# Optimization experiments

Hardware: AMD Instinct MI355X
Metric: run time of the kernel (lower is better)

Reference implementation:

```python
import jax, jax.numpy as jnp
import numpy as np
from jax import lax

S, B, VIN, VOUT, U, E = 64, 256, 128, 128, 1024, 512
START_CODE = 0
T_DEC = 25  # MAX_DECODE_STEPS


def gru_step(x, h, Wih, Whh, bih, bhh):
    # PyTorch GRU cell, gate order r,z,n
    gi = x @ Wih.T + bih
    gh = h @ Whh.T + bhh
    ir, iz, inn = jnp.split(gi, 3, axis=-1)
    hr, hz, hn = jnp.split(gh, 3, axis=-1)
    r = jax.nn.sigmoid(ir + hr)
    z = jax.nn.sigmoid(iz + hz)
    n = jnp.tanh(inn + r * hn)
    return (1.0 - z) * n + z * h


def setup_inputs() -> dict:
    key = jax.random.key(0)
    ks = jax.random.split(key, 20)
    sc = 0.05
    inp = {
        'x': jax.random.normal(ks[0], (S, B, VIN), jnp.float32),
        'x_len': jnp.maximum(jnp.sort(jax.random.randint(ks[1], (B,), 0, S + 1)), 1),
        'enc_Wih': jax.random.normal(ks[2], (3 * U, VIN), jnp.float32) * sc,
        'enc_Whh': jax.random.normal(ks[3], (3 * U, U), jnp.float32) * sc,
        'enc_bih': jnp.zeros((3 * U,), jnp.float32),
        'enc_bhh': jnp.zeros((3 * U,), jnp.float32),
        'dec_Wih': jax.random.normal(ks[4], (3 * U, E + U), jnp.float32) * sc,
        'dec_Whh': jax.random.normal(ks[5], (3 * U, U), jnp.float32) * sc,
        'dec_bih': jnp.zeros((3 * U,), jnp.float32),
        'dec_bhh': jnp.zeros((3 * U,), jnp.float32),
        'o2h_W': jax.random.normal(ks[6], (E, VOUT), jnp.float32) * sc,
        'o2h_b': jnp.zeros((E,), jnp.float32),
        'fc_W': jax.random.normal(ks[7], (VOUT, U), jnp.float32) * sc,
        'fc_b': jnp.zeros((VOUT,), jnp.float32),
        'W1_W': jax.random.normal(ks[8], (U, U), jnp.float32) * sc,
        'W1_b': jnp.zeros((U,), jnp.float32),
        'W2_W': jax.random.normal(ks[9], (U, U), jnp.float32) * sc,
        'W2_b': jnp.zeros((U,), jnp.float32),
        'V_W': jax.random.normal(ks[10], (1, U), jnp.float32) * sc,
        'V_b': jnp.zeros((1,), jnp.float32),
    }
    return inp


def _forward(x, x_len, enc_Wih, enc_Whh, enc_bih, enc_bhh,
             dec_Wih, dec_Whh, dec_bih, dec_bhh,
             o2h_W, o2h_b, fc_W, fc_b, W1_W, W1_b, W2_W, W2_b, V_W, V_b):
    # ---- Encoder GRU with length masking (pack/pad semantics) ----
    h0 = jnp.zeros((B, U), jnp.float32)
    t_idx = jnp.arange(S)

    def enc_step(h, inp_t):
        xt, t = inp_t
        mask = (t < x_len)[:, None]  # [B,1]
        hn = gru_step(xt, h, enc_Wih, enc_Whh, enc_bih, enc_bhh)
        h = jnp.where(mask, hn, h)
        out = jnp.where(mask, hn, 0.0)
        return h, out

    enc_hidden, enc_out = lax.scan(enc_step, h0, (x, t_idx))  # enc_out [S,B,U]
    enc_out = jnp.transpose(enc_out, (1, 0, 2))  # [B,S,U]

    # ---- Greedy decode (teacher_force=False), 25 steps ----
    enc_proj = enc_out @ W1_W.T + W1_b  # precompute W1(enc_output), [B,S,U]
    start = jnp.zeros((B, VOUT), jnp.float32).at[:, START_CODE].set(1.0)

    def dec_step(carry, _):
        h, dec_in = carry
        score = jnp.tanh(enc_proj + (h @ W2_W.T + W2_b)[:, None, :])  # [B,S,U]
        logits = score @ V_W.T + V_b  # [B,S,1]
        attn = jax.nn.softmax(logits, axis=1)
        ctx = jnp.sum(attn * enc_out, axis=1)  # [B,U]
        emb = dec_in @ o2h_W.T + o2h_b  # [B,E]
        gx = jnp.concatenate([ctx, emb], axis=-1)
        hn = gru_step(gx, h, dec_Wih, dec_Whh, dec_bih, dec_bhh)
        pred = hn @ fc_W.T + fc_b  # [B,VOUT]
        onehot = jax.nn.one_hot(jnp.argmax(pred, axis=-1), VOUT, dtype=pred.dtype)
        return (hn, lax.stop_gradient(onehot)), pred

    _, preds = lax.scan(dec_step, (enc_hidden, start), None, length=T_DEC - 1)
    return jnp.concatenate([start[None], preds], axis=0)  # [25,B,VOUT]


def reference(x, x_len, enc_Wih, enc_Whh, enc_bih, enc_bhh,
              dec_Wih, dec_Whh, dec_bih, dec_bhh,
              o2h_W, o2h_b, fc_W, fc_b, W1_W, W1_b, W2_W, W2_b, V_W, V_b):
    return _forward(x, x_len, enc_Wih, enc_Whh, enc_bih, enc_bhh,
                    dec_Wih, dec_Whh, dec_bih, dec_bhh,
                    o2h_W, o2h_b, fc_W, fc_b, W1_W, W1_b, W2_W, W2_b, V_W, V_b)
```

## Files before the change

### kernel.cpp

```cpp
#include <hip/hip_runtime.h>
#include <math.h>

#define SLEN 64
#define BATCH 256
#define VIND 128
#define VOUTD 128
#define UDIM 1024
#define EDIM 512
#define TDEC 25
#define GXW 1536
#define U3 3072
#define NSEG 12

typedef __attribute__((ext_vector_type(8))) short short8;
typedef __attribute__((ext_vector_type(4))) float f32x4;

#define MFMA(acc, A, B) acc = __builtin_amdgcn_mfma_f32_16x16x32_bf16((A), (B), (acc), 0, 0, 0)

__device__ __forceinline__ float sigm(float x) { return 1.f / (1.f + expf(-x)); }

__device__ __forceinline__ float tanhf_fast(float x) {
    float ax = fabsf(x);
    float e = __expf(-2.f * ax);
    float t = (1.f - e) / (1.f + e);
    return copysignf(t, x);
}

__device__ __forceinline__ short f2bf(float f) {
    unsigned u = __float_as_uint(f);
    u += 0x7FFF + ((u >> 16) & 1);
    return (short)(u >> 16);
}
__device__ __forceinline__ float bf2f(short h) {
    return __uint_as_float(((unsigned)(unsigned short)h) << 16);
}

__device__ __forceinline__ size_t pkChunk(int r, int k, int K) {
    return ((size_t)(r >> 4) * (K >> 5) + (k >> 5)) * 64 + ((r & 15) + 16 * ((k >> 3) & 3));
}

union S8 { short s[8]; short8 v; };

__device__ __forceinline__ void writeSplit8(short* Hi, short* Lo, size_t chunk,
                                            const float* vals) {
    S8 h, l;
#pragma unroll
    for (int j = 0; j < 8; j++) {
        short hb = f2bf(vals[j]);
        h.s[j] = hb;
        l.s[j] = f2bf(vals[j] - bf2f(hb));
    }
    ((short8*)Hi)[chunk] = h.v;
    ((short8*)Lo)[chunk] = l.v;
}

__global__ void init_kernel(float* __restrict__ h0, short* __restrict__ hpHi,
                            short* __restrict__ hpLo, float* __restrict__ out0,
                            int* __restrict__ idx,
                            const float* __restrict__ o2h_W,
                            const float* __restrict__ o2h_b,
                            float* __restrict__ o2hT) {
    int i = blockIdx.x * 256 + threadIdx.x;
    if (i < BATCH * UDIM) { h0[i] = 0.f; hpHi[i] = 0; hpLo[i] = 0; }
    if (i < BATCH * VOUTD) out0[i] = ((i & (VOUTD - 1)) == 0) ? 1.f : 0.f;
    if (i < BATCH) idx[i] = 0;
    if (i < VOUTD * EDIM) {
        int v = i >> 9, e = i & (EDIM - 1);
        o2hT[i] = o2h_W[(size_t)e * VOUTD + v] + o2h_b[e];
    }
}

struct PackSeg {
    const float* sA; const float* sB;
    short* Hi; short* Lo;
    int KA, KB, offA, offB, chunkStart;
};
struct PackArgs { PackSeg s[NSEG]; };

__global__ void pack_all(PackArgs pa, int total) {
    int gid = blockIdx.x * 256 + threadIdx.x;
    if (gid >= total) return;
    int si = 0;
#pragma unroll
    for (int i = 1; i < NSEG; i++) si = (gid >= pa.s[i].chunkStart) ? i : si;
    PackSeg sg = pa.s[si];
    int local = gid - sg.chunkStart;
    int K = sg.KA + sg.KB;
    int cpr = K >> 3;
    int r = local / cpr, k0 = (local - r * cpr) * 8;
    const float* src = (k0 < sg.KA)
        ? sg.sA + (size_t)(sg.offA + r) * sg.KA + k0
        : sg.sB + (size_t)(sg.offB + r) * sg.KB + (k0 - sg.KA);
    float v[8];
#pragma unroll
    for (int j = 0; j < 8; j++) v[j] = src[j];
    writeSplit8(sg.Hi, sg.Lo, pkChunk(r, k0, K), v);
}

__global__ __launch_bounds__(256) void gemm_w(
    const short8* __restrict__ Ahi, const short8* __restrict__ Alo,
    const short8* __restrict__ Whi, const short8* __restrict__ Wlo,
    const float* __restrict__ bias, float* __restrict__ C,
    int KT, int N) {
    int tid = threadIdx.x, lane = tid & 63, wave = tid >> 6;
    int m16 = blockIdx.x * 4 + (wave & 1) * 2;
    int nb = blockIdx.y * 8 + (wave >> 1) * 4;
    const short8* a0h = Ahi + (size_t)m16 * KT * 64 + lane;
    const short8* a1h = a0h + (size_t)KT * 64;
    const short8* a0l = Alo + (size_t)m16 * KT * 64 + lane;
    const short8* a1l = a0l + (size_t)KT * 64;
    const short8* w0h = Whi + (size_t)(nb + 0) * KT * 64 + lane;
    const short8* w1h = Whi + (size_t)(nb + 1) * KT * 64 + lane;
    const short8* w2h = Whi + (size_t)(nb + 2) * KT * 64 + lane;
    const short8* w3h = Whi + (size_t)(nb + 3) * KT * 64 + lane;
    const short8* w0l = Wlo + (size_t)(nb + 0) * KT * 64 + lane;
    const short8* w1l = Wlo + (size_t)(nb + 1) * KT * 64 + lane;
    const short8* w2l = Wlo + (size_t)(nb + 2) * KT * 64 + lane;
    const short8* w3l = Wlo + (size_t)(nb + 3) * KT * 64 + lane;
    f32x4 acc0[4] = {}, acc1[4] = {};

    for (int kt = 0; kt < KT; kt++) {
        size_t o = (size_t)kt * 64;
        short8 A0H = a0h[o], A1H = a1h[o], A0L = a0l[o], A1L = a1l[o];
        short8 WH0 = w0h[o], WL0 = w0l[o];
        MFMA(acc0[0], A0H, WH0); MFMA(acc1[0], A1H, WH0);
        MFMA(acc0[0], A0H, WL0); MFMA(acc1[0], A1H, WL0);
        MFMA(acc0[0], A0L, WH0); MFMA(acc1[0], A1L, WH0);
        short8 WH1 = w1h[o], WL1 = w1l[o];
        MFMA(acc0[1], A0H, WH1); MFMA(acc1[1], A1H, WH1);
        MFMA(acc0[1], A0H, WL1); MFMA(acc1[1], A1H, WL1);
        MFMA(acc0[1], A0L, WH1); MFMA(acc1[1], A1L, WH1);
        short8 WH2 = w2h[o], WL2 = w2l[o];
        MFMA(acc0[2], A0H, WH2); MFMA(acc1[2], A1H, WH2);
        MFMA(acc0[2], A0H, WL2); MFMA(acc1[2], A1H, WL2);
        MFMA(acc0[2], A0L, WH2); MFMA(acc1[2], A1L, WH2);
        short8 WH3 = w3h[o], WL3 = w3l[o];
        MFMA(acc0[3], A0H, WH3); MFMA(acc1[3], A1H, WH3);
        MFMA(acc0[3], A0H, WL3); MFMA(acc1[3], A1H, WL3);
        MFMA(acc0[3], A0L, WH3); MFMA(acc1[3], A1L, WH3);
    }
    int rsub = (lane >> 4) * 4, cn = lane & 15;
    int row0 = (m16 + 0) * 16 + rsub;
    int row1 = (m16 + 1) * 16 + rsub;
#pragma unroll
    for (int j = 0; j < 4; j++) {
        int col = (nb + j) * 16 + cn;
        float bb = bias ? bias[col] : 0.f;
#pragma unroll
        for (int r = 0; r < 4; r++) {
            C[(size_t)(row0 + r) * N + col] = acc0[j][r] + bb;
            C[(size_t)(row1 + r) * N + col] = acc1[j][r] + bb;
        }
    }
}

__global__ __launch_bounds__(256) void gemm_bm32(
    const short8* __restrict__ Ahi, const short8* __restrict__ Alo,
    const short8* __restrict__ Whi, const short8* __restrict__ Wlo,
    const float* __restrict__ bias, float* __restrict__ C,
    int KT, int N) {
    int tid = threadIdx.x, lane = tid & 63, wave = tid >> 6;
    int m16 = blockIdx.x * 2 + (wave & 1);
    int n16 = blockIdx.y * 4 + (wave >> 1) * 2;
    const short8* ah = Ahi + (size_t)m16 * KT * 64 + lane;
    const short8* al = Alo + (size_t)m16 * KT * 64 + lane;
    const short8* w0h = Whi + (size_t)n16 * KT * 64 + lane;
    const short8* w1h = w0h + (size_t)KT * 64;
    const short8* w0l = Wlo + (size_t)n16 * KT * 64 + lane;
    const short8* w1l = w0l + (size_t)KT * 64;
    f32x4 a0 = {0,0,0,0}, a1 = {0,0,0,0};
    for (int kt = 0; kt < KT; kt++) {
        size_t o = (size_t)kt * 64;
        short8 AH = ah[o], AL = al[o];
        short8 W0H = w0h[o], W0L = w0l[o], W1H = w1h[o], W1L = w1l[o];
        MFMA(a0, AH, W0H); MFMA(a1, AH, W1H);
        MFMA(a0, AH, W0L); MFMA(a1, AH, W1L);
        MFMA(a0, AL, W0H); MFMA(a1, AL, W1H);
    }
    int rsub = (lane >> 4) * 4, cn = lane & 15;
    float b0 = bias ? bias[(n16 + 0) * 16 + cn] : 0.f;
    float b1 = bias ? bias[(n16 + 1) * 16 + cn] : 0.f;
#pragma unroll
    for (int r = 0; r < 4; r++) {
        int row = m16 * 16 + rsub + r;
        C[(size_t)row * N + (n16 + 0) * 16 + cn] = a0[r] + b0;
        C[(size_t)row * N + (n16 + 1) * 16 + cn] = a1[r] + b1;
    }
}

__global__ __launch_bounds__(384) void enc_gru3(
    const short8* __restrict__ hinH8, const short8* __restrict__ hinL8,
    const short8* __restrict__ WrH, const short8* __restrict__ WrL,
    const short8* __restrict__ WzH, const short8* __restrict__ WzL,
    const short8* __restrict__ WnH, const short8* __restrict__ WnL,
    const float* __restrict__ gi,
    const float* __restrict__ bih, const float* __restrict__ bhh,
    const float* __restrict__ hinF, float* __restrict__ houtF,
    short* __restrict__ hoH, short* __restrict__ hoL,
    short* __restrict__ eaHi, short* __restrict__ eaLo,
    const int* __restrict__ x_len, int t) {
    __shared__ float sC[6][2][16][16];
    __shared__ float sHo[2][16][16];
    __shared__ float sEo[2][16][16];
    int tid = threadIdx.x, lane = tid & 63, wave = tid >> 6;
    int g = blockIdx.x;
    int m16a = blockIdx.y * 2;
    int gate = wave >> 1, half = wave & 1;
    const short8* a0h = hinH8 + (size_t)m16a * 32 * 64 + (size_t)half * 16 * 64 + lane;
    const short8* a0l = hinL8 + (size_t)m16a * 32 * 64 + (size_t)half * 16 * 64 + lane;
    const short8* a1h = a0h + (size_t)32 * 64;
    const short8* a1l = a0l + (size_t)32 * 64;
    const short8* WH0 = (gate == 0) ? WrH : (gate == 1) ? WzH : WnH;
    const short8* WL0 = (gate == 0) ? WrL : (gate == 1) ? WzL : WnL;
    const short8* wh = WH0 + (size_t)g * 32 * 64 + (size_t)half * 16 * 64 + lane;
    const short8* wl = WL0 + (size_t)g * 32 * 64 + (size_t)half * 16 * 64 + lane;
    f32x4 acc0 = {0, 0, 0, 0}, acc1 = {0, 0, 0, 0};
    for (int kt = 0; kt < 16; kt++) {
        size_t o = (size_t)kt * 64;
        short8 WH = wh[o], WL = wl[o];
        short8 A0H = a0h[o], A0L = a0l[o];
        MFMA(acc0, A0H, WH); MFMA(acc0, A0H, WL); MFMA(acc0, A0L, WH);
        short8 A1H = a1h[o], A1L = a1l[o];
        MFMA(acc1, A1H, WH); MFMA(acc1, A1H, WL); MFMA(acc1, A1L, WH);
    }
    {
        int rsub = (lane >> 4) << 2, cn = lane & 15;
#pragma unroll
        for (int j = 0; j < 4; j++) {
            sC[wave][0][rsub + j][cn] = acc0[j];
            sC[wave][1][rsub + j][cn] = acc1[j];
        }
    }
    __syncthreads();
    if (wave < 2) {
        int m16 = m16a + wave;
        int cu = g * 16 + (lane & 15);
        int rsub = (lane >> 4) << 2;
        float b_r = bih[cu] + bhh[cu];
        float b_z = bih[UDIM + cu] + bhh[UDIM + cu];
        float b_nh = bhh[2 * UDIM + cu];
        float b_ni = bih[2 * UDIM + cu];
        int growLocal = (t & 7) * 256;
#pragma unroll
        for (int j = 0; j < 4; j++) {
            int rr = rsub + j, cc = lane & 15;
            int b = m16 * 16 + rr;
            const float* gr = gi + (size_t)(growLocal + b) * U3;
            float rg = sigm(sC[0][wave][rr][cc] + sC[1][wave][rr][cc] + gr[cu] + b_r);
            float zg = sigm(sC[2][wave][rr][cc] + sC[3][wave][rr][cc] + gr[UDIM + cu] + b_z);
            float nn = tanhf(gr[2 * UDIM + cu] + b_ni +
                             rg * (sC[4][wave][rr][cc] + sC[5][wave][rr][cc] + b_nh));
            float hp = hinF[(size_t)b * UDIM + cu];
            float hv = (1.f - zg) * nn + zg * hp;
            bool msk = t < x_len[b];
            float ho = msk ? hv : hp;
            houtF[(size_t)b * UDIM + cu] = ho;
            sHo[wave][rr][cc] = ho;
            sEo[wave][rr][cc] = msk ? hv : 0.f;
        }
    }
    __syncthreads();
    if (wave >= 2 && wave < 4 && lane < 32) {
        int tile = wave - 2;
        int m16 = m16a + tile;
        int rr = lane >> 1, oct = lane & 1;
        int brow = m16 * 16 + rr;
        int u0 = g * 16 + oct * 8;
        float v[8];
#pragma unroll
        for (int j = 0; j < 8; j++) v[j] = sHo[tile][rr][oct * 8 + j];
        writeSplit8(hoH, hoL, pkChunk(brow, u0, UDIM), v);
#pragma unroll
        for (int j = 0; j < 8; j++) v[j] = sEo[tile][rr][oct * 8 + j];
        writeSplit8(eaHi, eaLo, pkChunk(brow * SLEN + t, u0, UDIM), v);
    }
}

__global__ __launch_bounds__(384) void dec_gru3(
    const short8* __restrict__ hinH8, const short8* __restrict__ hinL8,
    const short8* __restrict__ gxH8, const short8* __restrict__ gxL8,
    const short8* __restrict__ WrH, const short8* __restrict__ WrL,
    const short8* __restrict__ WzH, const short8* __restrict__ WzL,
    const short8* __restrict__ WnhH, const short8* __restrict__ WnhL,
    const short8* __restrict__ WniH, const short8* __restrict__ WniL,
    const float* __restrict__ bih, const float* __restrict__ bhh,
    const float* __restrict__ hinF, float* __restrict__ houtF,
    short* __restrict__ hoH, short* __restrict__ hoL) {
    __shared__ float sC[8][2][16][16];
    __shared__ float sHo[2][16][16];
    int tid = threadIdx.x, lane = tid & 63, wave = tid >> 6;
    int g = blockIdx.x;
    int m16a = blockIdx.y * 2;
    int gate = wave >> 1, half = wave & 1;
    const short8* a0h = hinH8 + (size_t)m16a * 32 * 64 + (size_t)half * 16 * 64 + lane;
    const short8* a0l = hinL8 + (size_t)m16a * 32 * 64 + (size_t)half * 16 * 64 + lane;
    const short8* a1h = a0h + (size_t)32 * 64;
    const short8* a1l = a0l + (size_t)32 * 64;
    const short8* g0h = gxH8 + (size_t)m16a * 48 * 64 + (size_t)half * 24 * 64 + lane;
    const short8* g0l = gxL8 + (size_t)m16a * 48 * 64 + (size_t)half * 24 * 64 + lane;
    const short8* g1h = g0h + (size_t)48 * 64;
    const short8* g1l = g0l + (size_t)48 * 64;
    const short8 *whA, *wlA, *whB, *wlB;
    if (gate == 0) {
        whA = WrH + (size_t)g * 80 * 64 + (size_t)half * 16 * 64 + lane;
        wlA = WrL + (size_t)g * 80 * 64 + (size_t)half * 16 * 64 + lane;
        whB = WrH + (size_t)g * 80 * 64 + (size_t)(32 + half * 24) * 64 + lane;
        wlB = WrL + (size_t)g * 80 * 64 + (size_t)(32 + half * 24) * 64 + lane;
    } else if (gate == 1) {
        whA = WzH + (size_t)g * 80 * 64 + (size_t)half * 16 * 64 + lane;
        wlA = WzL + (size_t)g * 80 * 64 + (size_t)half * 16 * 64 + lane;
        whB = WzH + (size_t)g * 80 * 64 + (size_t)(32 + half * 24) * 64 + lane;
        wlB = WzL + (size_t)g * 80 * 64 + (size_t)(32 + half * 24) * 64 + lane;
    } else {
        whA = WnhH + (size_t)g * 32 * 64 + (size_t)half * 16 * 64 + lane;
        wlA = WnhL + (size_t)g * 32 * 64 + (size_t)half * 16 * 64 + lane;
        whB = WniH + (size_t)g * 48 * 64 + (size_t)half * 24 * 64 + lane;
        wlB = WniL + (size_t)g * 48 * 64 + (size_t)half * 24 * 64 + lane;
    }
    f32x4 accA0 = {0,0,0,0}, accA1 = {0,0,0,0};
    f32x4 accB0 = {0,0,0,0}, accB1 = {0,0,0,0};
    for (int kt = 0; kt < 16; kt++) {
        size_t o = (size_t)kt * 64;
        short8 WH = whA[o], WL = wlA[o];
        short8 A0H = a0h[o], A0L = a0l[o];
        MFMA(accA0, A0H, WH); MFMA(accA0, A0H, WL); MFMA(accA0, A0L, WH);
        short8 A1H = a1h[o], A1L = a1l[o];
        MFMA(accA1, A1H, WH); MFMA(accA1, A1H, WL); MFMA(accA1, A1L, WH);
    }
    for (int kt = 0; kt < 24; kt++) {
        size_t o = (size_t)kt * 64;
        short8 WH = whB[o], WL = wlB[o];
        short8 G0H = g0h[o], G0L = g0l[o];
        MFMA(accB0, G0H, WH); MFMA(accB0, G0H, WL); MFMA(accB0, G0L, WH);
        short8 G1H = g1h[o], G1L = g1l[o];
        MFMA(accB1, G1H, WH); MFMA(accB1, G1H, WL); MFMA(accB1, G1L, WH);
    }
    {
        int rsub = (lane >> 4) << 2, cn = lane & 15;
        if (wave < 4) {
#pragma unroll
            for (int j = 0; j < 4; j++) {
                sC[wave][0][rsub + j][cn] = accA0[j] + accB0[j];
                sC[wave][1][rsub + j][cn] = accA1[j] + accB1[j];
            }
        } else {
#pragma unroll
            for (int j = 0; j < 4; j++) {
                sC[wave][0][rsub + j][cn] = accA0[j];
                sC[wave][1][rsub + j][cn] = accA1[j];
                sC[wave + 2][0][rsub + j][cn] = accB0[j];
                sC[wave + 2][1][rsub + j][cn] = accB1[j];
            }
        }
    }
    __syncthreads();
    if (wave < 2) {
        int m16 = m16a + wave;
        int cu = g * 16 + (lane & 15);
        int rsub = (lane >> 4) << 2;
        float b_r = bih[cu] + bhh[cu];
        float b_z = bih[UDIM + cu] + bhh[UDIM + cu];
        float b_nh = bhh[2 * UDIM + cu];
        float b_ni = bih[2 * UDIM + cu];
#pragma unroll
        for (int j = 0; j < 4; j++) {
            int rr = rsub + j, cc = lane & 15;
            int b = m16 * 16 + rr;
            float rg = sigm(sC[0][wave][rr][cc] + sC[1][wave][rr][cc] + b_r);
            float zg = sigm(sC[2][wave][rr][cc] + sC[3][wave][rr][cc] + b_z);
            float nn = tanhf(sC[6][wave][rr][cc] + sC[7][wave][rr][cc] + b_ni +
                             rg * (sC[4][wave][rr][cc] + sC[5][wave][rr][cc] + b_nh));
            float hp = hinF[(size_t)b * UDIM + cu];
            float hv = (1.f - zg) * nn + zg * hp;
            houtF[(size_t)b * UDIM + cu] = hv;
            sHo[wave][rr][cc] = hv;
        }
    }
    __syncthreads();
    if (wave >= 2 && wave < 4 && lane < 32) {
        int tile = wave - 2;
        int m16 = m16a + tile;
        int rr = lane >> 1, oct = lane & 1;
        int brow = m16 * 16 + rr;
        int u0 = g * 16 + oct * 8;
        float v[8];
#pragma unroll
        for (int j = 0; j < 8; j++) v[j] = sHo[tile][rr][oct * 8 + j];
        writeSplit8(hoH, hoL, pkChunk(brow, u0, UDIM), v);
    }
}

__global__ __launch_bounds__(1024) void attn_ctx(
    const float* __restrict__ encProj,
    const short* __restrict__ eaHi, const short* __restrict__ eaLo,
    const float* __restrict__ tmp2, const float* __restrict__ V_W,
    const float* __restrict__ V_b,
    const float* __restrict__ o2hT,
    const int* __restrict__ idx, short* __restrict__ gxHi, short* __restrict__ gxLo) {
    int b = blockIdx.x;
    int tid = threadIdx.x, lane = tid & 63, wave = tid >> 6;
    __shared__ float s_t2[UDIM];
    __shared__ float s_v[UDIM];
    __shared__ float s_attn[SLEN];
    __shared__ float s_part[7][128][9];
    for (int u = tid; u < UDIM; u += 1024) {
        s_t2[u] = tmp2[(size_t)b * UDIM + u];
        s_v[u] = V_W[u];
    }
    __syncthreads();
    for (int s = wave; s < SLEN; s += 16) {
        const float4* ep4 = (const float4*)(encProj + ((size_t)b * SLEN + s) * UDIM);
        float p = 0.f;
        for (int u4 = lane; u4 < UDIM / 4; u4 += 64) {
            float4 e = ep4[u4];
            int u = 4 * u4;
            p += tanhf_fast(e.x + s_t2[u]) * s_v[u] +
                 tanhf_fast(e.y + s_t2[u + 1]) * s_v[u + 1] +
                 tanhf_fast(e.z + s_t2[u + 2]) * s_v[u + 2] +
                 tanhf_fast(e.w + s_t2[u + 3]) * s_v[u + 3];
        }
#pragma unroll
        for (int off = 32; off > 0; off >>= 1) p += __shfl_xor(p, off);
        if (lane == 0) s_attn[s] = p + V_b[0];
    }
    __syncthreads();
    if (tid < 64) {
        float v = s_attn[tid];
        float mx = v;
#pragma unroll
        for (int off = 32; off > 0; off >>= 1) mx = fmaxf(mx, __shfl_xor(mx, off));
        float e = expf(v - mx);
        float sum = e;
#pragma unroll
        for (int off = 32; off > 0; off >>= 1) sum += __shfl_xor(sum, off);
        s_attn[tid] = e / sum;
    }
    __syncthreads();
    {
        int grp = tid >> 7, tu = tid & 127;
        int u0 = tu * 8;
        float a[8] = {0, 0, 0, 0, 0, 0, 0, 0};
        const short8* hi8 = (const short8*)eaHi;
        const short8* lo8 = (const short8*)eaLo;
        int lanePart = 16 * ((u0 >> 3) & 3);
        int colPart = u0 >> 5;
        for (int s = grp * 8; s < grp * 8 + 8; s++) {
            int r = b * SLEN + s;
            size_t ch = ((size_t)(r >> 4) * (UDIM >> 5) + colPart) * 64 + (r & 15) + lanePart;
            S8 h, l;
            h.v = hi8[ch];
            l.v = lo8[ch];
            float w = s_attn[s];
#pragma unroll
            for (int j = 0; j < 8; j++) a[j] += w * (bf2f(h.s[j]) + bf2f(l.s[j]));
        }
        if (grp) {
#pragma unroll
            for (int j = 0; j < 8; j++) s_part[grp - 1][tu][j] = a[j];
        }
        __syncthreads();
        if (tid < 128) {
#pragma unroll
            for (int gg = 0; gg < 7; gg++)
#pragma unroll
                for (int j = 0; j < 8; j++) a[j] += s_part[gg][tu][j];
            writeSplit8(gxHi, gxLo, pkChunk(b, u0, GXW), a);
        } else if (tid < 192) {
            int e0 = (tid - 128) * 8;
            int ib = idx[b];
            const float* row = o2hT + (size_t)ib * EDIM + e0;
            float v[8];
#pragma unroll
            for (int j = 0; j < 8; j++) v[j] = row[j];
            writeSplit8(gxHi, gxLo, pkChunk(b, UDIM + e0, GXW), v);
        }
    }
}

__global__ __launch_bounds__(256) void fcw2(
    const short8* __restrict__ hHi, const short8* __restrict__ hLo,
    const short8* __restrict__ fcH, const short8* __restrict__ fcL,
    const float* __restrict__ fc_b, float* __restrict__ pred,
    int* __restrict__ idx,
    const short8* __restrict__ w2H, const short8* __restrict__ w2L,
    const float* __restrict__ W2_b, float* __restrict__ tmp2) {
    __shared__ float sP[16][129];
    int tid = threadIdx.x, lane = tid & 63, wave = tid >> 6;
    if (blockIdx.x < 16) {
        int fm = blockIdx.x;
        const short8* ah = hHi + (size_t)fm * 32 * 64 + lane;
        const short8* al = hLo + (size_t)fm * 32 * 64 + lane;
        int n0 = 2 * wave, n1 = 2 * wave + 1;
        const short8* w0h = fcH + (size_t)n0 * 32 * 64 + lane;
        const short8* w0l = fcL + (size_t)n0 * 32 * 64 + lane;
        const short8* w1h = fcH + (size_t)n1 * 32 * 64 + lane;
        const short8* w1l = fcL + (size_t)n1 * 32 * 64 + lane;
        f32x4 a0 = {0,0,0,0}, a1 = {0,0,0,0};
        for (int kt = 0; kt < 32; kt++) {
            size_t o = (size_t)kt * 64;
            short8 AH = ah[o], AL = al[o];
            short8 W0H = w0h[o], W0L = w0l[o], W1H = w1h[o], W1L = w1l[o];
            MFMA(a0, AH, W0H); MFMA(a1, AH, W1H);
            MFMA(a0, AH, W0L); MFMA(a1, AH, W1L);
            MFMA(a0, AL, W0H); MFMA(a1, AL, W1H);
        }
        int cn = lane & 15, rsub = (lane >> 4) << 2;
#pragma unroll
        for (int j = 0; j < 4; j++) {
            sP[rsub + j][n0 * 16 + cn] = a0[j] + fc_b[n0 * 16 + cn];
            sP[rsub + j][n1 * 16 + cn] = a1[j] + fc_b[n1 * 16 + cn];
        }
        __syncthreads();
        {
            int row = tid >> 4, c0 = (tid & 15) * 8;
            float* pr = pred + (size_t)(fm * 16 + row) * VOUTD;
#pragma unroll
            for (int j = 0; j < 8; j++) pr[c0 + j] = sP[row][c0 + j];
        }
        if (tid < 128) {
            int row = tid >> 3, seg = tid & 7;
            float v = -1e30f;
            int bi = 0;
            int c0 = seg * 16;
            for (int j = c0; j < c0 + 16; j++) {
                float w = sP[row][j];
                if (w > v) { v = w; bi = j; }
            }
#pragma unroll
            for (int off = 1; off < 8; off <<= 1) {
                float ov = __shfl_xor(v, off);
                int obi = __shfl_xor(bi, off);
                if (ov > v || (ov == v && obi < bi)) { v = ov; bi = obi; }
            }
            if (seg == 0) idx[fm * 16 + row] = bi;
        }
    } else {
        int lin = blockIdx.x - 16;
        int bx = lin & 7, by = lin >> 3;
        int m16 = bx * 2 + (wave & 1);
        int n16 = by * 4 + (wave >> 1) * 2;
        const short8* ah = hHi + (size_t)m16 * 32 * 64 + lane;
        const short8* al = hLo + (size_t)m16 * 32 * 64 + lane;
        const short8* w0h = w2H + (size_t)n16 * 32 * 64 + lane;
        const short8* w1h = w0h + (size_t)32 * 64;
        const short8* w0l = w2L + (size_t)n16 * 32 * 64 + lane;
        const short8* w1l = w0l + (size_t)32 * 64;
        f32x4 a0 = {0,0,0,0}, a1 = {0,0,0,0};
        for (int kt = 0; kt < 32; kt++) {
            size_t o = (size_t)kt * 64;
            short8 AH = ah[o], AL = al[o];
            short8 W0H = w0h[o], W0L = w0l[o], W1H = w1h[o], W1L = w1l[o];
            MFMA(a0, AH, W0H); MFMA(a1, AH, W1H);
            MFMA(a0, AH, W0L); MFMA(a1, AH, W1L);
            MFMA(a0, AL, W0H); MFMA(a1, AL, W1H);
        }
        int rsub = (lane >> 4) * 4, cn = lane & 15;
        float b0 = W2_b[(n16 + 0) * 16 + cn];
        float b1 = W2_b[(n16 + 1) * 16 + cn];
#pragma unroll
        for (int r = 0; r < 4; r++) {
            int row = m16 * 16 + rsub + r;
            tmp2[(size_t)row * UDIM + (n16 + 0) * 16 + cn] = a0[r] + b0;
            tmp2[(size_t)row * UDIM + (n16 + 1) * 16 + cn] = a1[r] + b1;
        }
    }
}

extern "C" void kernel_launch(void* const* d_in, const int* in_sizes, int n_in,
                              void* d_out, int out_size, void* d_ws, size_t ws_size,
                              hipStream_t stream) {
    const float* x       = (const float*)d_in[0];
    const int*   x_len   = (const int*)d_in[1];
    const float* enc_Wih = (const float*)d_in[2];
    const float* enc_Whh = (const float*)d_in[3];
    const float* enc_bih = (const float*)d_in[4];
    const float* enc_bhh = (const float*)d_in[5];
    const float* dec_Wih = (const float*)d_in[6];
    const float* dec_Whh = (const float*)d_in[7];
    const float* dec_bih = (const float*)d_in[8];
    const float* dec_bhh = (const float*)d_in[9];
    const float* o2h_W   = (const float*)d_in[10];
    const float* o2h_b   = (const float*)d_in[11];
    const float* fc_W    = (const float*)d_in[12];
    const float* fc_b    = (const float*)d_in[13];
    const float* W1_W    = (const float*)d_in[14];
    const float* W1_b    = (const float*)d_in[15];
    const float* W2_W    = (const float*)d_in[16];
    const float* W2_b    = (const float*)d_in[17];
    const float* V_W     = (const float*)d_in[18];
    const float* V_b     = (const float*)d_in[19];
    float* out = (float*)d_out;

    char* p = (char*)d_ws;
    auto alloc = [&](size_t bytes) -> char* {
        char* q = p;
        p += (bytes + 255) & ~(size_t)255;
        return q;
    };
    float* hAF  = (float*)alloc((size_t)BATCH * UDIM * 4);
    float* hBF  = (float*)alloc((size_t)BATCH * UDIM * 4);
    short* hAH  = (short*)alloc((size_t)BATCH * UDIM * 2);
    short* hAL  = (short*)alloc((size_t)BATCH * UDIM * 2);
    short* hBH  = (short*)alloc((size_t)BATCH * UDIM * 2);
    short* hBL  = (short*)alloc((size_t)BATCH * UDIM * 2);
    float* tmp2 = (float*)alloc((size_t)BATCH * UDIM * 4);
    short* gxHi = (short*)alloc((size_t)BATCH * GXW * 2);
    short* gxLo = (short*)alloc((size_t)BATCH * GXW * 2);
    short* encAHi = (short*)alloc((size_t)BATCH * SLEN * UDIM * 2);
    short* encALo = (short*)alloc((size_t)BATCH * SLEN * UDIM * 2);
    float* encProjF = (float*)alloc((size_t)BATCH * SLEN * UDIM * 4);
    float* gihBuf = (float*)alloc((size_t)8 * BATCH * U3 * 4);
    short* eWihH = (short*)alloc((size_t)U3 * VIND * 2);
    short* eWihL = (short*)alloc((size_t)U3 * VIND * 2);
    short* eWrH = (short*)alloc((size_t)UDIM * UDIM * 2);
    short* eWrL = (short*)alloc((size_t)UDIM * UDIM * 2);
    short* eWzH = (short*)alloc((size_t)UDIM * UDIM * 2);
    short* eWzL = (short*)alloc((size_t)UDIM * UDIM * 2);
    short* eWnH = (short*)alloc((size_t)UDIM * UDIM * 2);
    short* eWnL = (short*)alloc((size_t)UDIM * UDIM * 2);
    short* dWrH = (short*)alloc((size_t)UDIM * 2560 * 2);
    short* dWrL = (short*)alloc((size_t)UDIM * 2560 * 2);
    short* dWzH = (short*)alloc((size_t)UDIM * 2560 * 2);
    short* dWzL = (short*)alloc((size_t)UDIM * 2560 * 2);
    short* dWnhH = (short*)alloc((size_t)UDIM * UDIM * 2);
    short* dWnhL = (short*)alloc((size_t)UDIM * UDIM * 2);
    short* dWniH = (short*)alloc((size_t)UDIM * GXW * 2);
    short* dWniL = (short*)alloc((size_t)UDIM * GXW * 2);
    short* w1Hi = (short*)alloc((size_t)UDIM * UDIM * 2);
    short* w1Lo = (short*)alloc((size_t)UDIM * UDIM * 2);
    short* w2Hi = (short*)alloc((size_t)UDIM * UDIM * 2);
    short* w2Lo = (short*)alloc((size_t)UDIM * UDIM * 2);
    short* fcHi = (short*)alloc((size_t)VOUTD * UDIM * 2);
    short* fcLo = (short*)alloc((size_t)VOUTD * UDIM * 2);
    short* xHi  = (short*)alloc((size_t)SLEN * BATCH * VIND * 2);
    short* xLo  = (short*)alloc((size_t)SLEN * BATCH * VIND * 2);
    int*   idx  = (int*)alloc(BATCH * 4);
    float* o2hT = (float*)alloc((size_t)VOUTD * EDIM * 4);

    init_kernel<<<(BATCH * UDIM + 255) / 256, 256, 0, stream>>>(
        hAF, hAH, hAL, out, idx, o2h_W, o2h_b, o2hT);

    {
        PackArgs pa;
        int cs = 0, n = 0;
        auto seg = [&](const float* sA, int KA, int offA, const float* sB, int KB,
                       int offB, short* Hi, short* Lo, int R) {
            pa.s[n] = {sA, sB, Hi, Lo, KA, KB, offA, offB, cs};
            cs += R * (KA + KB) / 8;
            n++;
        };
        seg(enc_Wih, VIND, 0, nullptr, 0, 0, eWihH, eWihL, U3);
        seg(enc_Whh, UDIM, 0, nullptr, 0, 0, eWrH, eWrL, UDIM);
        seg(enc_Whh, UDIM, UDIM, nullptr, 0, 0, eWzH, eWzL, UDIM);
        seg(enc_Whh, UDIM, 2 * UDIM, nullptr, 0, 0, eWnH, eWnL, UDIM);
        seg(dec_Whh, UDIM, 0, dec_Wih, GXW, 0, dWrH, dWrL, UDIM);
        seg(dec_Whh, UDIM, UDIM, dec_Wih, GXW, UDIM, dWzH, dWzL, UDIM);
        seg(dec_Whh, UDIM, 2 * UDIM, nullptr, 0, 0, dWnhH, dWnhL, UDIM);
        seg(dec_Wih, GXW, 2 * UDIM, nullptr, 0, 0, dWniH, dWniL, UDIM);
        seg(W1_W, UDIM, 0, nullptr, 0, 0, w1Hi, w1Lo, UDIM);
        seg(W2_W, UDIM, 0, nullptr, 0, 0, w2Hi, w2Lo, UDIM);
        seg(fc_W, UDIM, 0, nullptr, 0, 0, fcHi, fcLo, VOUTD);
        seg(x, VIND, 0, nullptr, 0, 0, xHi, xLo, SLEN * BATCH);
        pack_all<<<(cs + 255) / 256, 256, 0, stream>>>(pa, cs);
    }

    float* hcF = hAF; float* hnF = hBF;
    short *hcH = hAH, *hcL = hAL, *hnH = hBH, *hnL = hBL;
    for (int c = 0; c < 8; c++) {
        gemm_w<<<dim3(32, 24), 256, 0, stream>>>(
            (const short8*)xHi + (size_t)c * 128 * 4 * 64,
            (const short8*)xLo + (size_t)c * 128 * 4 * 64,
            (const short8*)eWihH, (const short8*)eWihL,
            nullptr, gihBuf, VIND / 32, U3);
        for (int tt = 0; tt < 8; tt++) {
            int t = c * 8 + tt;
            enc_gru3<<<dim3(64, 8), 384, 0, stream>>>(
                (const short8*)hcH, (const short8*)hcL,
                (const short8*)eWrH, (const short8*)eWrL,
                (const short8*)eWzH, (const short8*)eWzL,
                (const short8*)eWnH, (const short8*)eWnL,
                gihBuf, enc_bih, enc_bhh, hcF, hnF, hnH, hnL,
                encAHi, encALo, x_len, t);
            { float* tf = hcF; hcF = hnF; hnF = tf; }
            { short* th = hcH; hcH = hnH; hnH = th; th = hcL; hcL = hnL; hnL = th; }
        }
    }

    gemm_w<<<dim3(SLEN * BATCH / 64, UDIM / 128), 256, 0, stream>>>(
        (const short8*)encAHi, (const short8*)encALo,
        (const short8*)w1Hi, (const short8*)w1Lo,
        W1_b, encProjF, UDIM / 32, UDIM);

    gemm_bm32<<<dim3(BATCH / 32, UDIM / 64), 256, 0, stream>>>(
        (const short8*)hcH, (const short8*)hcL,
        (const short8*)w2Hi, (const short8*)w2Lo,
        W2_b, tmp2, UDIM / 32, UDIM);

    for (int st = 0; st < TDEC - 1; st++) {
        attn_ctx<<<BATCH, 1024, 0, stream>>>(
            encProjF, encAHi, encALo, tmp2, V_W, V_b, o2hT, idx, gxHi, gxLo);
        dec_gru3<<<dim3(64, 8), 384, 0, stream>>>(
            (const short8*)hcH, (const short8*)hcL,
            (const short8*)gxHi, (const short8*)gxLo,
            (const short8*)dWrH, (const short8*)dWrL,
            (const short8*)dWzH, (const short8*)dWzL,
            (const short8*)dWnhH, (const short8*)dWnhL,
            (const short8*)dWniH, (const short8*)dWniL,
            dec_bih, dec_bhh, hcF, hnF, hnH, hnL);
        float* pred = out + (size_t)(1 + st) * BATCH * VOUTD;
        fcw2<<<144, 256, 0, stream>>>(
            (const short8*)hnH, (const short8*)hnL,
            (const short8*)fcHi, (const short8*)fcLo,
            fc_b, pred, idx,
            (const short8*)w2Hi, (const short8*)w2Lo, W2_b, tmp2);
        { float* tf = hcF; hcF = hnF; hnF = tf; }
        { short* th = hcH; hcH = hnH; hnH = th; th = hcL; hcL = hnL; hnL = th; }
    }
}
```

Baseline: 3.487 ms.

## Double batch tile per block in encoder and decoder GRU step kernels

```diff
diff --git a/kernel.cpp b/kernel.cpp
--- a/kernel.cpp
+++ b/kernel.cpp
@@ -188,7 +188,7 @@
     }
 }
 
-__global__ __launch_bounds__(384) void enc_gru3(
+__global__ __launch_bounds__(768) void enc_gru3(
     const short8* __restrict__ hinH8, const short8* __restrict__ hinL8,
     const short8* __restrict__ WrH, const short8* __restrict__ WrL,
     const short8* __restrict__ WzH, const short8* __restrict__ WzL,
@@ -199,15 +199,16 @@
     short* __restrict__ hoH, short* __restrict__ hoL,
     short* __restrict__ eaHi, short* __restrict__ eaLo,
     const int* __restrict__ x_len, int t) {
-    __shared__ float sC[6][2][16][16];
-    __shared__ float sHo[2][16][16];
-    __shared__ float sEo[2][16][16];
+    __shared__ float sC[6][4][16][16];
+    __shared__ float sHo[4][16][16];
+    __shared__ float sEo[4][16][16];
     int tid = threadIdx.x, lane = tid & 63, wave = tid >> 6;
     int g = blockIdx.x;
-    int m16a = blockIdx.y * 2;
-    int gate = wave >> 1, half = wave & 1;
-    const short8* a0h = hinH8 + (size_t)m16a * 32 * 64 + (size_t)half * 16 * 64 + lane;
-    const short8* a0l = hinL8 + (size_t)m16a * 32 * 64 + (size_t)half * 16 * 64 + lane;
+    int m16a = blockIdx.y * 4;
+    int gate = wave >> 2, hm = wave & 3, half = hm >> 1, mp = hm & 1;
+    int t0 = mp * 2;
+    const short8* a0h = hinH8 + (size_t)(m16a + t0) * 32 * 64 + (size_t)half * 16 * 64 + lane;
+    const short8* a0l = hinL8 + (size_t)(m16a + t0) * 32 * 64 + (size_t)half * 16 * 64 + lane;
     const short8* a1h = a0h + (size_t)32 * 64;
     const short8* a1l = a0l + (size_t)32 * 64;
     const short8* WH0 = (gate == 0) ? WrH : (gate == 1) ? WzH : WnH;
@@ -224,16 +225,18 @@
         MFMA(acc1, A1H, WH); MFMA(acc1, A1H, WL); MFMA(acc1, A1L, WH);
     }
     {
+        int slot = gate * 2 + half;
         int rsub = (lane >> 4) << 2, cn = lane & 15;
 #pragma unroll
         for (int j = 0; j < 4; j++) {
-            sC[wave][0][rsub + j][cn] = acc0[j];
-            sC[wave][1][rsub + j][cn] = acc1[j];
+            sC[slot][t0 + 0][rsub + j][cn] = acc0[j];
+            sC[slot][t0 + 1][rsub + j][cn] = acc1[j];
         }
     }
     __syncthreads();
-    if (wave < 2) {
-        int m16 = m16a + wave;
+    if (wave < 4) {
+        int tile = wave;
+        int m16 = m16a + tile;
         int cu = g * 16 + (lane & 15);
         int rsub = (lane >> 4) << 2;
         float b_r = bih[cu] + bhh[cu];
@@ -246,22 +249,22 @@
             int rr = rsub + j, cc = lane & 15;
             int b = m16 * 16 + rr;
             const float* gr = gi + (size_t)(growLocal + b) * U3;
-            float rg = sigm(sC[0][wave][rr][cc] + sC[1][wave][rr][cc] + gr[cu] + b_r);
-            float zg = sigm(sC[2][wave][rr][cc] + sC[3][wave][rr][cc] + gr[UDIM + cu] + b_z);
+            float rg = sigm(sC[0][tile][rr][cc] + sC[1][tile][rr][cc] + gr[cu] + b_r);
+            float zg = sigm(sC[2][tile][rr][cc] + sC[3][tile][rr][cc] + gr[UDIM + cu] + b_z);
             float nn = tanhf(gr[2 * UDIM + cu] + b_ni +
-                             rg * (sC[4][wave][rr][cc] + sC[5][wave][rr][cc] + b_nh));
+                             rg * (sC[4][tile][rr][cc] + sC[5][tile][rr][cc] + b_nh));
             float hp = hinF[(size_t)b * UDIM + cu];
             float hv = (1.f - zg) * nn + zg * hp;
             bool msk = t < x_len[b];
             float ho = msk ? hv : hp;
             houtF[(size_t)b * UDIM + cu] = ho;
-            sHo[wave][rr][cc] = ho;
-            sEo[wave][rr][cc] = msk ? hv : 0.f;
+            sHo[tile][rr][cc] = ho;
+            sEo[tile][rr][cc] = msk ? hv : 0.f;
         }
     }
     __syncthreads();
-    if (wave >= 2 && wave < 4 && lane < 32) {
-        int tile = wave - 2;
+    if (wave >= 4 && wave < 8 && lane < 32) {
+        int tile = wave - 4;
         int m16 = m16a + tile;
         int rr = lane >> 1, oct = lane & 1;
         int brow = m16 * 16 + rr;
@@ -276,7 +279,7 @@
     }
 }
 
-__global__ __launch_bounds__(384) void dec_gru3(
+__global__ __launch_bounds__(768) void dec_gru3(
     const short8* __restrict__ hinH8, const short8* __restrict__ hinL8,
     const short8* __restrict__ gxH8, const short8* __restrict__ gxL8,
     const short8* __restrict__ WrH, const short8* __restrict__ WrL,
@@ -286,18 +289,19 @@
     const float* __restrict__ bih, const float* __restrict__ bhh,
     const float* __restrict__ hinF, float* __restrict__ houtF,
     short* __restrict__ hoH, short* __restrict__ hoL) {
-    __shared__ float sC[8][2][16][16];
-    __shared__ float sHo[2][16][16];
+    __shared__ float sC[8][4][16][16];
+    __shared__ float sHo[4][16][16];
     int tid = threadIdx.x, lane = tid & 63, wave = tid >> 6;
     int g = blockIdx.x;
-    int m16a = blockIdx.y * 2;
-    int gate = wave >> 1, half = wave & 1;
-    const short8* a0h = hinH8 + (size_t)m16a * 32 * 64 + (size_t)half * 16 * 64 + lane;
-    const short8* a0l = hinL8 + (size_t)m16a * 32 * 64 + (size_t)half * 16 * 64 + lane;
+    int m16a = blockIdx.y * 4;
+    int gate = wave >> 2, hm = wave & 3, half = hm >> 1, mp = hm & 1;
+    int t0 = mp * 2;
+    const short8* a0h = hinH8 + (size_t)(m16a + t0) * 32 * 64 + (size_t)half * 16 * 64 + lane;
+    const short8* a0l = hinL8 + (size_t)(m16a + t0) * 32 * 64 + (size_t)half * 16 * 64 + lane;
     const short8* a1h = a0h + (size_t)32 * 64;
     const short8* a1l = a0l + (size_t)32 * 64;
-    const short8* g0h = gxH8 + (size_t)m16a * 48 * 64 + (size_t)half * 24 * 64 + lane;
-    const short8* g0l = gxL8 + (size_t)m16a * 48 * 64 + (size_t)half * 24 * 64 + lane;
+    const short8* g0h = gxH8 + (size_t)(m16a + t0) * 48 * 64 + (size_t)half * 24 * 64 + lane;
+    const short8* g0l = gxL8 + (size_t)(m16a + t0) * 48 * 64 + (size_t)half * 24 * 64 + lane;
     const short8* g1h = g0h + (size_t)48 * 64;
     const short8* g1l = g0l + (size_t)48 * 64;
     const short8 *whA, *wlA, *whB, *wlB;
@@ -337,25 +341,27 @@
     }
     {
         int rsub = (lane >> 4) << 2, cn = lane & 15;
-        if (wave < 4) {
+        if (gate < 2) {
+            int slot = gate * 2 + half;
 #pragma unroll
             for (int j = 0; j < 4; j++) {
-                sC[wave][0][rsub + j][cn] = accA0[j] + accB0[j];
-                sC[wave][1][rsub + j][cn] = accA1[j] + accB1[j];
+                sC[slot][t0 + 0][rsub + j][cn] = accA0[j] + accB0[j];
+                sC[slot][t0 + 1][rsub + j][cn] = accA1[j] + accB1[j];
             }
         } else {
 #pragma unroll
             for (int j = 0; j < 4; j++) {
-                sC[wave][0][rsub + j][cn] = accA0[j];
-                sC[wave][1][rsub + j][cn] = accA1[j];
-                sC[wave + 2][0][rsub + j][cn] = accB0[j];
-                sC[wave + 2][1][rsub + j][cn] = accB1[j];
+                sC[4 + half][t0 + 0][rsub + j][cn] = accA0[j];
+                sC[4 + half][t0 + 1][rsub + j][cn] = accA1[j];
+                sC[6 + half][t0 + 0][rsub + j][cn] = accB0[j];
+                sC[6 + half][t0 + 1][rsub + j][cn] = accB1[j];
             }
         }
     }
     __syncthreads();
-    if (wave < 2) {
-        int m16 = m16a + wave;
+    if (wave < 4) {
+        int tile = wave;
+        int m16 = m16a + tile;
         int cu = g * 16 + (lane & 15);
         int rsub = (lane >> 4) << 2;
         float b_r = bih[cu] + bhh[cu];
@@ -366,19 +372,19 @@
         for (int j = 0; j < 4; j++) {
             int rr = rsub + j, cc = lane & 15;
             int b = m16 * 16 + rr;
-            float rg = sigm(sC[0][wave][rr][cc] + sC[1][wave][rr][cc] + b_r);
-            float zg = sigm(sC[2][wave][rr][cc] + sC[3][wave][rr][cc] + b_z);
-            float nn = tanhf(sC[6][wave][rr][cc] + sC[7][wave][rr][cc] + b_ni +
-                             rg * (sC[4][wave][rr][cc] + sC[5][wave][rr][cc] + b_nh));
+            float rg = sigm(sC[0][tile][rr][cc] + sC[1][tile][rr][cc] + b_r);
+            float zg = sigm(sC[2][tile][rr][cc] + sC[3][tile][rr][cc] + b_z);
+            float nn = tanhf(sC[6][tile][rr][cc] + sC[7][tile][rr][cc] + b_ni +
+                             rg * (sC[4][tile][rr][cc] + sC[5][tile][rr][cc] + b_nh));
             float hp = hinF[(size_t)b * UDIM + cu];
             float hv = (1.f - zg) * nn + zg * hp;
             houtF[(size_t)b * UDIM + cu] = hv;
-            sHo[wave][rr][cc] = hv;
+            sHo[tile][rr][cc] = hv;
         }
     }
     __syncthreads();
-    if (wave >= 2 && wave < 4 && lane < 32) {
-        int tile = wave - 2;
+    if (wave >= 4 && wave < 8 && lane < 32) {
+        int tile = wave - 4;
         int m16 = m16a + tile;
         int rr = lane >> 1, oct = lane & 1;
         int brow = m16 * 16 + rr;
@@ -674,7 +680,7 @@
             nullptr, gihBuf, VIND / 32, U3);
         for (int tt = 0; tt < 8; tt++) {
             int t = c * 8 + tt;
-            enc_gru3<<<dim3(64, 8), 384, 0, stream>>>(
+            enc_gru3<<<dim3(64, 4), 768, 0, stream>>>(
                 (const short8*)hcH, (const short8*)hcL,
                 (const short8*)eWrH, (const short8*)eWrL,
                 (const short8*)eWzH, (const short8*)eWzL,
@@ -699,7 +705,7 @@
     for (int st = 0; st < TDEC - 1; st++) {
         attn_ctx<<<BATCH, 1024, 0, stream>>>(
             encProjF, encAHi, encALo, tmp2, V_W, V_b, o2hT, idx, gxHi, gxLo);
-        dec_gru3<<<dim3(64, 8), 384, 0, stream>>>(
+        dec_gru3<<<dim3(64, 4), 768, 0, stream>>>(
             (const short8*)hcH, (const short8*)hcL,
             (const short8*)gxHi, (const short8*)gxLo,
             (const short8*)dWrH, (const short8*)dWrL,
```

Result: no change. 3.464 ms (-0.7%).
